# Performance work log

Measured on AMD Instinct MI355X. Metric: run time of the kernel, lower is better.

The kernel has to match this reference:

```python
import jax, jax.numpy as jnp
import numpy as np

B, S, H, NH, DH, FF = 8, 512, 768, 12, 64, 3072
EPS = 1e-3  # matches epsilon used in the repo's LayerNormalization


def layer_norm(x, g, b):
    mu = jnp.mean(x, axis=-1, keepdims=True)
    var = jnp.mean(jnp.square(x - mu), axis=-1, keepdims=True)
    return (x - mu) * jax.lax.rsqrt(var + EPS) * g + b


def setup_inputs() -> dict:
    key = jax.random.key(0)
    ks = jax.random.split(key, 12)
    init = lambda k, shp: (jax.random.normal(k, shp, dtype=jnp.float32) * 0.02)
    return {
        "hidden_states": jax.random.normal(ks[0], (B, S, H), dtype=jnp.float32),
        "attention_mask": jnp.ones((B, S), dtype=jnp.int32),
        "Wq": init(ks[1], (H, H)), "bq": jnp.zeros((H,), jnp.float32),
        "Wk": init(ks[2], (H, H)), "bk": jnp.zeros((H,), jnp.float32),
        "Wv": init(ks[3], (H, H)), "bv": jnp.zeros((H,), jnp.float32),
        "Wo": init(ks[4], (H, H)), "bo": jnp.zeros((H,), jnp.float32),
        "ln1_g": jnp.ones((H,), jnp.float32), "ln1_b": jnp.zeros((H,), jnp.float32),
        "W1": init(ks[5], (H, FF)), "b1": jnp.zeros((FF,), jnp.float32),
        "W2": init(ks[6], (FF, H)), "b2": jnp.zeros((H,), jnp.float32),
        "ln2_g": jnp.ones((H,), jnp.float32), "ln2_b": jnp.zeros((H,), jnp.float32),
    }


def reference(hidden_states, attention_mask, Wq, bq, Wk, bk, Wv, bv, Wo, bo,
              ln1_g, ln1_b, W1, b1, W2, b2, ln2_g, ln2_b):
    x = hidden_states  # [B,S,H]
    b, s, h = x.shape
    split = lambda t: t.reshape(b, s, NH, DH).transpose(0, 2, 1, 3)  # [B,NH,S,DH]
    q = split(x @ Wq + bq)
    k = split(x @ Wk + bk)
    v = split(x @ Wv + bv)
    scores = jnp.einsum("bhqd,bhkd->bhqk", q, k) / jnp.sqrt(jnp.float32(DH))
    # BERT-style additive mask: (1 - mask) * -10000, broadcast over heads/queries
    m = attention_mask.astype(jnp.float32)[:, None, None, :]
    scores = scores + (1.0 - m) * -10000.0
    probs = jax.nn.softmax(scores, axis=-1)
    ctx = jnp.einsum("bhqk,bhkd->bhqd", probs, v)
    ctx = ctx.transpose(0, 2, 1, 3).reshape(b, s, h)  # [B,S,H]
    attn_out = ctx @ Wo + bo
    h1 = layer_norm(attn_out + x, ln1_g, ln1_b)
    ff = jax.nn.gelu(h1 @ W1 + b1, approximate=False) @ W2 + b2
    return layer_norm(ff + h1, ln2_g, ln2_b)
```

## Files before the change

kernel.cpp:

```cpp
#include <hip/hip_runtime.h>
#include <hip/hip_bf16.h>

#define H_DIM 768
#define FF_DIM 3072
#define NHEAD 12
#define DHEAD 64
#define SEQ 512
#define TOK 4096

typedef __bf16 bf16;
using bf16x8 = __attribute__((ext_vector_type(8))) __bf16;
using f32x4  = __attribute__((ext_vector_type(4))) float;

static __device__ __forceinline__ f32x4 mfma16(bf16x8 a, bf16x8 b, f32x4 c) {
  return __builtin_amdgcn_mfma_f32_16x16x32_bf16(a, b, c, 0, 0, 0);
}

static __device__ __forceinline__ void gl2lds16(const bf16* g, bf16* l) {
  __builtin_amdgcn_global_load_lds((const __attribute__((address_space(1))) void*)g,
                                   (__attribute__((address_space(3))) void*)l, 16, 0, 0);
}

__global__ __launch_bounds__(256) void cvt_k(const float* __restrict__ in, bf16* __restrict__ out, int n) {
  int i = (blockIdx.x * 256 + threadIdx.x) * 8;
  if (i >= n) return;
  float4 a = *(const float4*)(in + i);
  float4 b = *(const float4*)(in + i + 4);
  bf16x8 o;
  o[0] = (bf16)a.x; o[1] = (bf16)a.y; o[2] = (bf16)a.z; o[3] = (bf16)a.w;
  o[4] = (bf16)b.x; o[5] = (bf16)b.y; o[6] = (bf16)b.z; o[7] = (bf16)b.w;
  *(bf16x8*)(out + i) = o;
}

__global__ __launch_bounds__(256) void cvtT_k(const float* __restrict__ in, bf16* __restrict__ out,
                                              int R, int C) {
  __shared__ bf16 tile[32][33];
  int c0 = blockIdx.x * 32, r0 = blockIdx.y * 32;
  int tx = threadIdx.x & 31, ty = threadIdx.x >> 5;
  for (int i = 0; i < 32; i += 8) tile[ty + i][tx] = (bf16)in[(size_t)(r0 + ty + i) * C + c0 + tx];
  __syncthreads();
  for (int i = 0; i < 32; i += 8) out[(size_t)(c0 + ty + i) * R + r0 + tx] = tile[tx][ty + i];
}

struct GemmArgs {
  const bf16* A;
  const bf16* W[3];
  const float* bias[3];
  bf16* outB[3];
  float* outP[2];
  int N, K, nx, ry, kSlices;
};

#define BK 32

template <int MODE>
__global__ __launch_bounds__(256) void gemm_x(GemmArgs args) {
  __shared__ bf16 As[128 * BK];
  __shared__ bf16 Bs[128 * BK];
  int bid = blockIdx.x;
  int xcd = bid & 7, tt = bid >> 3;
  int ry = args.ry;
  int by = xcd * ry + (tt % ry);
  int rest = tt / ry;
  int bx = rest % args.nx;
  int z = rest / args.nx;

  const bf16* A = args.A;
  const bf16* Bt;
  int Kd = args.K, N = args.N;
  int kBeg, kEnd;
  if constexpr (MODE == 2) {
    Bt = args.W[0];
    int ks = Kd / args.kSlices;
    kBeg = z * ks; kEnd = kBeg + ks;
  } else {
    Bt = args.W[z];
    kBeg = 0; kEnd = Kd;
  }
  int m0 = by * 128, n0 = bx * 128;
  int t = threadIdx.x;
  int wid = t >> 6, lane = t & 63, quad = lane >> 4, l16 = lane & 15;
  int wm = wid >> 1, wn = wid & 1;

  f32x4 zero4 = {0.0f, 0.0f, 0.0f, 0.0f};
  f32x4 acc[4][4];
#pragma unroll
  for (int mi = 0; mi < 4; mi++)
#pragma unroll
    for (int ni = 0; ni < 4; ni++) acc[mi][ni] = zero4;

  int ch = wid * 2;
  int rA = lane >> 2;
  int cE = (lane & 3) * 8;
  const bf16* gA0 = A  + (size_t)(m0 + ch * 16 + rA) * Kd + cE;
  const bf16* gA1 = gA0 + (size_t)16 * Kd;
  const bf16* gB0 = Bt + (size_t)(n0 + ch * 16 + rA) * Kd + cE;
  const bf16* gB1 = gB0 + (size_t)16 * Kd;
  bf16* lA0 = As + ch * 512;
  bf16* lA1 = As + ch * 512 + 512;
  bf16* lB0 = Bs + ch * 512;
  bf16* lB1 = Bs + ch * 512 + 512;

  for (int k0 = kBeg; k0 < kEnd; k0 += BK) {
    __syncthreads();
    gl2lds16(gA0 + k0, lA0);
    gl2lds16(gA1 + k0, lA1);
    gl2lds16(gB0 + k0, lB0);
    gl2lds16(gB1 + k0, lB1);
    __syncthreads();
    bf16x8 af[4], bfr[4];
#pragma unroll
    for (int mi = 0; mi < 4; mi++) af[mi] = *(const bf16x8*)&As[(wm * 64 + mi * 16 + l16) * BK + quad * 8];
#pragma unroll
    for (int ni = 0; ni < 4; ni++) bfr[ni] = *(const bf16x8*)&Bs[(wn * 64 + ni * 16 + l16) * BK + quad * 8];
#pragma unroll
    for (int mi = 0; mi < 4; mi++)
#pragma unroll
      for (int ni = 0; ni < 4; ni++) acc[mi][ni] = mfma16(af[mi], bfr[ni], acc[mi][ni]);
  }

  if constexpr (MODE == 2) {
    float* outP = args.outP[z];
#pragma unroll
    for (int mi = 0; mi < 4; mi++) {
#pragma unroll
      for (int r = 0; r < 4; r++) {
        int row = m0 + wm * 64 + mi * 16 + quad * 4 + r;
#pragma unroll
        for (int ni = 0; ni < 4; ni++) {
          int col = n0 + wn * 64 + ni * 16 + l16;
          outP[(size_t)row * N + col] = acc[mi][ni][r];
        }
      }
    }
  } else {
    const float* bias = args.bias[z];
    bf16* outB = args.outB[z];
    float bv[4];
#pragma unroll
    for (int ni = 0; ni < 4; ni++) bv[ni] = bias[n0 + wn * 64 + ni * 16 + l16];
#pragma unroll
    for (int mi = 0; mi < 4; mi++) {
#pragma unroll
      for (int r = 0; r < 4; r++) {
        int row = m0 + wm * 64 + mi * 16 + quad * 4 + r;
#pragma unroll
        for (int ni = 0; ni < 4; ni++) {
          int col = n0 + wn * 64 + ni * 16 + l16;
          float v = acc[mi][ni][r] + bv[ni];
          if constexpr (MODE == 1) v = 0.5f * v * (1.0f + erff(v * 0.70710678118654752f));
          outB[(size_t)row * N + col] = (bf16)v;
        }
      }
    }
  }
}

#define CHK 128
#define LPAD 40
__global__ __launch_bounds__(256) void attn_k(const bf16* __restrict__ Qg, const bf16* __restrict__ Kg,
                                              const bf16* __restrict__ Vg, const int* __restrict__ mask,
                                              bf16* __restrict__ ctx) {
  __shared__ bf16 Ks[CHK][72];
  __shared__ bf16 Vts[DHEAD][CHK + 8];
  __shared__ float maskadd[CHK];
  __shared__ bf16 Ps[4][16][LPAD];
  int bh = blockIdx.y;
  int b = bh / NHEAD, h = bh % NHEAD;
  int q0 = blockIdx.x * 64;
  int t = threadIdx.x;
  int wid = t >> 6, lane = t & 63, quad = lane >> 4, l16 = lane & 15;
  size_t base = (size_t)b * SEQ * H_DIM + (size_t)h * DHEAD;

  int qrow = q0 + wid * 16 + l16;
  bf16x8 qf0 = *(const bf16x8*)(Qg + base + (size_t)qrow * H_DIM + quad * 8);
  bf16x8 qf1 = *(const bf16x8*)(Qg + base + (size_t)qrow * H_DIM + 32 + quad * 8);

  f32x4 zero4 = {0.0f, 0.0f, 0.0f, 0.0f};
  f32x4 o[4];
  float m_i[4], l_i[4];
#pragma unroll
  for (int r = 0; r < 4; r++) { o[r] = zero4; m_i[r] = -1e30f; l_i[r] = 0.0f; }

  for (int c0 = 0; c0 < SEQ; c0 += CHK) {
    __syncthreads();
    {
      int row = t >> 1, half = (t & 1) * 32;
      const bf16* g = Kg + base + (size_t)(c0 + row) * H_DIM + half;
      *(bf16x8*)&Ks[row][half]      = *(const bf16x8*)g;
      *(bf16x8*)&Ks[row][half + 8]  = *(const bf16x8*)(g + 8);
      *(bf16x8*)&Ks[row][half + 16] = *(const bf16x8*)(g + 16);
      *(bf16x8*)&Ks[row][half + 24] = *(const bf16x8*)(g + 24);
    }
#pragma unroll
    for (int pass = 0; pass < 4; ++pass) {
      int s = (t >> 3) + pass * 32, dg = (t & 7) * 8;
      bf16x8 v = *(const bf16x8*)(Vg + base + (size_t)(c0 + s) * H_DIM + dg);
#pragma unroll
      for (int j = 0; j < 8; j++) Vts[dg + j][s] = v[j];
    }
    if (t < CHK) maskadd[t] = (1.0f - (float)mask[b * SEQ + c0 + t]) * -10000.0f;
    __syncthreads();

    for (int kt = 0; kt < CHK; kt += 32) {
      f32x4 s0 = zero4, s1 = zero4;
      bf16x8 k0a = *(const bf16x8*)&Ks[kt + l16][quad * 8];
      bf16x8 k0b = *(const bf16x8*)&Ks[kt + l16][32 + quad * 8];
      bf16x8 k1a = *(const bf16x8*)&Ks[kt + 16 + l16][quad * 8];
      bf16x8 k1b = *(const bf16x8*)&Ks[kt + 16 + l16][32 + quad * 8];
      s0 = mfma16(qf0, k0a, s0); s0 = mfma16(qf1, k0b, s0);
      s1 = mfma16(qf0, k1a, s1); s1 = mfma16(qf1, k1b, s1);
      float add0 = maskadd[kt + l16], add1 = maskadd[kt + 16 + l16];
#pragma unroll
      for (int r = 0; r < 4; r++) {
        float v0 = s0[r] * 0.125f + add0;
        float v1 = s1[r] * 0.125f + add1;
        float mx = fmaxf(v0, v1);
#pragma unroll
        for (int off = 1; off < 16; off <<= 1) mx = fmaxf(mx, __shfl_xor(mx, off));
        float mnew = fmaxf(m_i[r], mx);
        float p0 = __expf(v0 - mnew), p1 = __expf(v1 - mnew);
        float alpha = __expf(m_i[r] - mnew);
        m_i[r] = mnew;
        float ps = p0 + p1;
#pragma unroll
        for (int off = 1; off < 16; off <<= 1) ps += __shfl_xor(ps, off);
        l_i[r] = l_i[r] * alpha + ps;
#pragma unroll
        for (int ni = 0; ni < 4; ni++) o[ni][r] *= alpha;
        Ps[wid][quad * 4 + r][l16]      = (bf16)p0;
        Ps[wid][quad * 4 + r][16 + l16] = (bf16)p1;
      }
      bf16x8 pa = *(const bf16x8*)&Ps[wid][l16][quad * 8];
#pragma unroll
      for (int ni = 0; ni < 4; ni++) {
        bf16x8 vb = *(const bf16x8*)&Vts[ni * 16 + l16][kt + quad * 8];
        o[ni] = mfma16(pa, vb, o[ni]);
      }
    }
  }
#pragma unroll
  for (int r = 0; r < 4; r++) {
    int row = q0 + wid * 16 + quad * 4 + r;
    float inv = 1.0f / l_i[r];
#pragma unroll
    for (int ni = 0; ni < 4; ni++)
      ctx[base + (size_t)row * H_DIM + ni * 16 + l16] = (bf16)(o[ni][r] * inv);
  }
}

__global__ __launch_bounds__(256) void redln_k(const float* __restrict__ p0, const float* __restrict__ p1,
                                               const float* __restrict__ resF, const bf16* __restrict__ resB,
                                               const float* __restrict__ bias,
                                               const float* __restrict__ g, const float* __restrict__ bta,
                                               bf16* __restrict__ outB, float* __restrict__ outF) {
  int row = blockIdx.x, t = threadIdx.x;
  size_t base = (size_t)row * H_DIM;
  float v[3], s = 0.0f, sq = 0.0f;
#pragma unroll
  for (int i = 0; i < 3; i++) {
    int c = t + i * 256;
    float r = resF ? resF[base + c] : (float)resB[base + c];
    float x = p0[base + c] + p1[base + c] + bias[c] + r;
    v[i] = x; s += x; sq += x * x;
  }
#pragma unroll
  for (int off = 32; off >= 1; off >>= 1) { s += __shfl_down(s, off); sq += __shfl_down(sq, off); }
  __shared__ float ssum[4], ssq[4], smu, srs;
  int lane = t & 63, w = t >> 6;
  if (lane == 0) { ssum[w] = s; ssq[w] = sq; }
  __syncthreads();
  if (t == 0) {
    float S = ssum[0] + ssum[1] + ssum[2] + ssum[3];
    float Q = ssq[0] + ssq[1] + ssq[2] + ssq[3];
    float mu = S * (1.0f / H_DIM);
    float var = Q * (1.0f / H_DIM) - mu * mu;
    smu = mu;
    srs = rsqrtf(var + 1e-3f);
  }
  __syncthreads();
  float mu = smu, rs = srs;
#pragma unroll
  for (int i = 0; i < 3; i++) {
    int c = t + i * 256;
    float y = (v[i] - mu) * rs * g[c] + bta[c];
    if (outB) outB[base + c] = (bf16)y;
    if (outF) outF[base + c] = y;
  }
}

extern "C" void kernel_launch(void* const* d_in, const int* in_sizes, int n_in,
                              void* d_out, int out_size, void* d_ws, size_t ws_size,
                              hipStream_t stream) {
  const float* x    = (const float*)d_in[0];
  const int*   mask = (const int*)d_in[1];
  const float* Wq = (const float*)d_in[2];  const float* bq = (const float*)d_in[3];
  const float* Wk = (const float*)d_in[4];  const float* bk = (const float*)d_in[5];
  const float* Wv = (const float*)d_in[6];  const float* bv = (const float*)d_in[7];
  const float* Wo = (const float*)d_in[8];  const float* bo = (const float*)d_in[9];
  const float* ln1g = (const float*)d_in[10]; const float* ln1b = (const float*)d_in[11];
  const float* W1 = (const float*)d_in[12]; const float* b1 = (const float*)d_in[13];
  const float* W2 = (const float*)d_in[14]; const float* b2 = (const float*)d_in[15];
  const float* ln2g = (const float*)d_in[16]; const float* ln2b = (const float*)d_in[17];
  float* out = (float*)d_out;
  (void)ws_size; (void)in_sizes; (void)n_in; (void)out_size;

  char* w = (char*)d_ws;
  const size_t SZ_TH  = 6291456;
  const size_t SZ_THF = 12582912;
  const size_t SZ_W   = 1179648;
  const size_t SZ_WF  = 4718592;
  bf16* xB   = (bf16*)(w);
  bf16* QB   = (bf16*)(w + SZ_TH);
  bf16* KB   = (bf16*)(w + 2 * SZ_TH);
  bf16* VB   = (bf16*)(w + 3 * SZ_TH);
  float* P1s0 = (float*)(w);
  float* P1s1 = (float*)(w + SZ_THF);
  bf16* FFA  = (bf16*)(w);
  bf16* CTX  = (bf16*)(w + 4 * SZ_TH);
  bf16* H1   = CTX;
  bf16* WqT  = (bf16*)(w + 5 * SZ_TH);
  bf16* WkT  = (bf16*)(w + 5 * SZ_TH + SZ_W);
  bf16* WvT  = (bf16*)(w + 5 * SZ_TH + 2 * SZ_W);
  bf16* WoT  = (bf16*)(w + 5 * SZ_TH + 3 * SZ_W);
  bf16* W1T  = (bf16*)(w + 5 * SZ_TH + 4 * SZ_W);
  float* P2s0 = (float*)(w + 5 * SZ_TH);
  float* P2s1 = (float*)(w + 5 * SZ_TH + SZ_THF);
  bf16* W2T  = (bf16*)(w + 5 * SZ_TH + 2 * SZ_THF);

  dim3 tb(256);

  cvt_k<<<(TOK * H_DIM) / 2048, tb, 0, stream>>>(x, xB, TOK * H_DIM);
  cvtT_k<<<dim3(24, 24), tb, 0, stream>>>(Wq, WqT, H_DIM, H_DIM);
  cvtT_k<<<dim3(24, 24), tb, 0, stream>>>(Wk, WkT, H_DIM, H_DIM);
  cvtT_k<<<dim3(24, 24), tb, 0, stream>>>(Wv, WvT, H_DIM, H_DIM);
  cvtT_k<<<dim3(24, 24), tb, 0, stream>>>(Wo, WoT, H_DIM, H_DIM);
  cvtT_k<<<dim3(96, 24), tb, 0, stream>>>(W1, W1T, H_DIM, FF_DIM);
  cvtT_k<<<dim3(24, 96), tb, 0, stream>>>(W2, W2T, FF_DIM, H_DIM);

  GemmArgs ga = {};
  ga.A = xB; ga.N = H_DIM; ga.K = H_DIM; ga.nx = 6; ga.ry = 4; ga.kSlices = 1;
  ga.W[0] = WqT; ga.W[1] = WkT; ga.W[2] = WvT;
  ga.bias[0] = bq; ga.bias[1] = bk; ga.bias[2] = bv;
  ga.outB[0] = QB; ga.outB[1] = KB; ga.outB[2] = VB;
  gemm_x<0><<<576, tb, 0, stream>>>(ga);

  attn_k<<<dim3(SEQ / 64, 8 * NHEAD), tb, 0, stream>>>(QB, KB, VB, mask, CTX);

  GemmArgs go = {};
  go.A = CTX; go.N = H_DIM; go.K = H_DIM; go.nx = 6; go.ry = 4; go.kSlices = 2;
  go.W[0] = WoT; go.outP[0] = P1s0; go.outP[1] = P1s1;
  gemm_x<2><<<384, tb, 0, stream>>>(go);

  redln_k<<<TOK, tb, 0, stream>>>(P1s0, P1s1, x, nullptr, bo, ln1g, ln1b, H1, nullptr);

  GemmArgs g1 = {};
  g1.A = H1; g1.N = FF_DIM; g1.K = H_DIM; g1.nx = 24; g1.ry = 4; g1.kSlices = 1;
  g1.W[0] = W1T; g1.bias[0] = b1; g1.outB[0] = FFA;
  gemm_x<1><<<768, tb, 0, stream>>>(g1);

  GemmArgs g2 = {};
  g2.A = FFA; g2.N = H_DIM; g2.K = FF_DIM; g2.nx = 6; g2.ry = 4; g2.kSlices = 2;
  g2.W[0] = W2T; g2.outP[0] = P2s0; g2.outP[1] = P2s1;
  gemm_x<2><<<384, tb, 0, stream>>>(g2);

  redln_k<<<TOK, tb, 0, stream>>>(P2s0, P2s1, nullptr, H1, b2, ln2g, ln2b, nullptr, out);
}
```

Baseline: 309.5 us.

## Restructure attention softmax per 128-key chunk and pack V transpose as key pairs

The attention kernel now computes all scores for a 128-key chunk before doing one online-softmax update per chunk, replacing one update every 32 keys. This cuts the number of cross-lane max/sum shuffles and the rescales of the output accumulator. The V transpose into LDS now packs two consecutive keys into each 32-bit word, which reduces scattered 16-bit LDS stores. The grid is also swapped so that batch-head varies fastest, and the four square weight transposes are batched into a single launch. These changes raise register and LDS pressure, since eight score tiles and a wider P buffer are now held at once.

```diff
diff --git a/kernel.cpp b/kernel.cpp
--- a/kernel.cpp
+++ b/kernel.cpp
@@ -32,9 +32,11 @@
   *(bf16x8*)(out + i) = o;
 }
 
-__global__ __launch_bounds__(256) void cvtT_k(const float* __restrict__ in, bf16* __restrict__ out,
-                                              int R, int C) {
+struct CvtTArgs { const float* in[4]; bf16* out[4]; };
+__global__ __launch_bounds__(256) void cvtT_k(CvtTArgs args, int R, int C) {
   __shared__ bf16 tile[32][33];
+  const float* in = args.in[blockIdx.z];
+  bf16* out = args.out[blockIdx.z];
   int c0 = blockIdx.x * 32, r0 = blockIdx.y * 32;
   int tx = threadIdx.x & 31, ty = threadIdx.x >> 5;
   for (int i = 0; i < 32; i += 8) tile[ty + i][tx] = (bf16)in[(size_t)(r0 + ty + i) * C + c0 + tx];
@@ -157,17 +159,16 @@
 }
 
 #define CHK 128
-#define LPAD 40
 __global__ __launch_bounds__(256) void attn_k(const bf16* __restrict__ Qg, const bf16* __restrict__ Kg,
                                               const bf16* __restrict__ Vg, const int* __restrict__ mask,
                                               bf16* __restrict__ ctx) {
   __shared__ bf16 Ks[CHK][72];
-  __shared__ bf16 Vts[DHEAD][CHK + 8];
+  __shared__ unsigned int Vts[DHEAD][68];
   __shared__ float maskadd[CHK];
-  __shared__ bf16 Ps[4][16][LPAD];
-  int bh = blockIdx.y;
+  __shared__ bf16 Ps[4][16][136];
+  int bh = blockIdx.x;
   int b = bh / NHEAD, h = bh % NHEAD;
-  int q0 = blockIdx.x * 64;
+  int q0 = blockIdx.y * 64;
   int t = threadIdx.x;
   int wid = t >> 6, lane = t & 63, quad = lane >> 4, l16 = lane & 15;
   size_t base = (size_t)b * SEQ * H_DIM + (size_t)h * DHEAD;
@@ -193,49 +194,63 @@
       *(bf16x8*)&Ks[row][half + 24] = *(const bf16x8*)(g + 24);
     }
 #pragma unroll
-    for (int pass = 0; pass < 4; ++pass) {
-      int s = (t >> 3) + pass * 32, dg = (t & 7) * 8;
-      bf16x8 v = *(const bf16x8*)(Vg + base + (size_t)(c0 + s) * H_DIM + dg);
-#pragma unroll
-      for (int j = 0; j < 8; j++) Vts[dg + j][s] = v[j];
+    for (int p = 0; p < 2; ++p) {
+      int kp = t & 63;
+      int dg = ((t >> 6) + p * 4) * 8;
+      const bf16* vp = Vg + base + (size_t)(c0 + 2 * kp) * H_DIM + dg;
+      bf16x8 v0 = *(const bf16x8*)vp;
+      bf16x8 v1 = *(const bf16x8*)(vp + H_DIM);
+      const unsigned short* u0 = (const unsigned short*)&v0;
+      const unsigned short* u1 = (const unsigned short*)&v1;
+#pragma unroll
+      for (int j = 0; j < 8; j++)
+        Vts[dg + j][kp] = (unsigned int)u0[j] | ((unsigned int)u1[j] << 16);
     }
     if (t < CHK) maskadd[t] = (1.0f - (float)mask[b * SEQ + c0 + t]) * -10000.0f;
     __syncthreads();
 
+    f32x4 sc[8];
+#pragma unroll
+    for (int k8 = 0; k8 < 8; k8++) {
+      const bf16* krow = &Ks[k8 * 16 + l16][0];
+      bf16x8 ka = *(const bf16x8*)(krow + quad * 8);
+      bf16x8 kb = *(const bf16x8*)(krow + 32 + quad * 8);
+      f32x4 s = mfma16(qf0, ka, zero4);
+      sc[k8] = mfma16(qf1, kb, s);
+    }
+    float madd[8];
+#pragma unroll
+    for (int k8 = 0; k8 < 8; k8++) madd[k8] = maskadd[k8 * 16 + l16];
+
+#pragma unroll
+    for (int r = 0; r < 4; r++) {
+      float v[8], mx = -1e30f;
+#pragma unroll
+      for (int k8 = 0; k8 < 8; k8++) { v[k8] = sc[k8][r] * 0.125f + madd[k8]; mx = fmaxf(mx, v[k8]); }
+#pragma unroll
+      for (int off = 1; off < 16; off <<= 1) mx = fmaxf(mx, __shfl_xor(mx, off));
+      float mnew = fmaxf(m_i[r], mx);
+      float alpha = __expf(m_i[r] - mnew);
+      m_i[r] = mnew;
+      float ps = 0.0f;
+#pragma unroll
+      for (int k8 = 0; k8 < 8; k8++) { v[k8] = __expf(v[k8] - mnew); ps += v[k8]; }
+#pragma unroll
+      for (int off = 1; off < 16; off <<= 1) ps += __shfl_xor(ps, off);
+      l_i[r] = l_i[r] * alpha + ps;
+#pragma unroll
+      for (int ni = 0; ni < 4; ni++) o[ni][r] *= alpha;
+#pragma unroll
+      for (int k8 = 0; k8 < 8; k8++) Ps[wid][quad * 4 + r][k8 * 16 + l16] = (bf16)v[k8];
+    }
+
+#pragma unroll
     for (int kt = 0; kt < CHK; kt += 32) {
-      f32x4 s0 = zero4, s1 = zero4;
-      bf16x8 k0a = *(const bf16x8*)&Ks[kt + l16][quad * 8];
-      bf16x8 k0b = *(const bf16x8*)&Ks[kt + l16][32 + quad * 8];
-      bf16x8 k1a = *(const bf16x8*)&Ks[kt + 16 + l16][quad * 8];
-      bf16x8 k1b = *(const bf16x8*)&Ks[kt + 16 + l16][32 + quad * 8];
-      s0 = mfma16(qf0, k0a, s0); s0 = mfma16(qf1, k0b, s0);
-      s1 = mfma16(qf0, k1a, s1); s1 = mfma16(qf1, k1b, s1);
-      float add0 = maskadd[kt + l16], add1 = maskadd[kt + 16 + l16];
-#pragma unroll
-      for (int r = 0; r < 4; r++) {
-        float v0 = s0[r] * 0.125f + add0;
-        float v1 = s1[r] * 0.125f + add1;
-        float mx = fmaxf(v0, v1);
-#pragma unroll
-        for (int off = 1; off < 16; off <<= 1) mx = fmaxf(mx, __shfl_xor(mx, off));
-        float mnew = fmaxf(m_i[r], mx);
-        float p0 = __expf(v0 - mnew), p1 = __expf(v1 - mnew);
-        float alpha = __expf(m_i[r] - mnew);
-        m_i[r] = mnew;
-        float ps = p0 + p1;
-#pragma unroll
-        for (int off = 1; off < 16; off <<= 1) ps += __shfl_xor(ps, off);
-        l_i[r] = l_i[r] * alpha + ps;
-#pragma unroll
-        for (int ni = 0; ni < 4; ni++) o[ni][r] *= alpha;
-        Ps[wid][quad * 4 + r][l16]      = (bf16)p0;
-        Ps[wid][quad * 4 + r][16 + l16] = (bf16)p1;
-      }
-      bf16x8 pa = *(const bf16x8*)&Ps[wid][l16][quad * 8];
+      bf16x8 pa = *(const bf16x8*)&Ps[wid][l16][kt + quad * 8];
 #pragma unroll
       for (int ni = 0; ni < 4; ni++) {
-        bf16x8 vb = *(const bf16x8*)&Vts[ni * 16 + l16][kt + quad * 8];
-        o[ni] = mfma16(pa, vb, o[ni]);
+        const bf16* vrow = (const bf16*)&Vts[ni * 16 + l16][0] + kt + quad * 8;
+        o[ni] = mfma16(pa, *(const bf16x8*)vrow, o[ni]);
       }
     }
   }
@@ -309,7 +324,6 @@
   const size_t SZ_TH  = 6291456;
   const size_t SZ_THF = 12582912;
   const size_t SZ_W   = 1179648;
-  const size_t SZ_WF  = 4718592;
   bf16* xB   = (bf16*)(w);
   bf16* QB   = (bf16*)(w + SZ_TH);
   bf16* KB   = (bf16*)(w + 2 * SZ_TH);
@@ -331,12 +345,14 @@
   dim3 tb(256);
 
   cvt_k<<<(TOK * H_DIM) / 2048, tb, 0, stream>>>(x, xB, TOK * H_DIM);
-  cvtT_k<<<dim3(24, 24), tb, 0, stream>>>(Wq, WqT, H_DIM, H_DIM);
-  cvtT_k<<<dim3(24, 24), tb, 0, stream>>>(Wk, WkT, H_DIM, H_DIM);
-  cvtT_k<<<dim3(24, 24), tb, 0, stream>>>(Wv, WvT, H_DIM, H_DIM);
-  cvtT_k<<<dim3(24, 24), tb, 0, stream>>>(Wo, WoT, H_DIM, H_DIM);
-  cvtT_k<<<dim3(96, 24), tb, 0, stream>>>(W1, W1T, H_DIM, FF_DIM);
-  cvtT_k<<<dim3(24, 96), tb, 0, stream>>>(W2, W2T, FF_DIM, H_DIM);
+  CvtTArgs ct = {};
+  ct.in[0] = Wq; ct.in[1] = Wk; ct.in[2] = Wv; ct.in[3] = Wo;
+  ct.out[0] = WqT; ct.out[1] = WkT; ct.out[2] = WvT; ct.out[3] = WoT;
+  cvtT_k<<<dim3(24, 24, 4), tb, 0, stream>>>(ct, H_DIM, H_DIM);
+  CvtTArgs c1 = {}; c1.in[0] = W1; c1.out[0] = W1T;
+  cvtT_k<<<dim3(96, 24, 1), tb, 0, stream>>>(c1, H_DIM, FF_DIM);
+  CvtTArgs c2 = {}; c2.in[0] = W2; c2.out[0] = W2T;
+  cvtT_k<<<dim3(24, 96, 1), tb, 0, stream>>>(c2, FF_DIM, H_DIM);
 
   GemmArgs ga = {};
   ga.A = xB; ga.N = H_DIM; ga.K = H_DIM; ga.nx = 6; ga.ry = 4; ga.kSlices = 1;
@@ -345,7 +361,7 @@
   ga.outB[0] = QB; ga.outB[1] = KB; ga.outB[2] = VB;
   gemm_x<0><<<576, tb, 0, stream>>>(ga);
 
-  attn_k<<<dim3(SEQ / 64, 8 * NHEAD), tb, 0, stream>>>(QB, KB, VB, mask, CTX);
+  attn_k<<<dim3(8 * NHEAD, SEQ / 64), tb, 0, stream>>>(QB, KB, VB, mask, CTX);
 
   GemmArgs go = {};
   go.A = CTX; go.N = H_DIM; go.K = H_DIM; go.nx = 6; go.ry = 4; go.kSlices = 2;
```

After: 286.0 us. -7.6%, faster.
